# Kernel tuning notes

Measured on AMD Instinct MI355X. Metric: run time of the kernel, lower is better.

The kernel has to match this reference:

```python
import jax, jax.numpy as jnp
import numpy as np
from jax import lax

DIM = 512
HEADS = 8
N = 2048
B = 4
EPS = 1e-12  # torch F.normalize eps


def setup_inputs() -> dict:
    key = jax.random.key(0)
    ks = jax.random.split(key, 8)
    s = 0.02
    return {
        "x": jax.random.normal(ks[0], (B, DIM, N), jnp.float32),
        "w_qkv": jax.random.normal(ks[1], (3 * DIM, DIM, 1), jnp.float32) * s,
        "b_qkv": jax.random.normal(ks[2], (3 * DIM,), jnp.float32) * s,
        "w_dw": jax.random.normal(ks[3], (3 * DIM, 1, 3), jnp.float32) * s,
        "b_dw": jax.random.normal(ks[4], (3 * DIM,), jnp.float32) * s,
        "w_po": jax.random.normal(ks[5], (DIM, DIM, 1), jnp.float32) * s,
        "b_po": jax.random.normal(ks[6], (DIM,), jnp.float32) * s,
        "temperature": jnp.ones((HEADS, 1, 1), jnp.float32),
    }


def _l2norm(x, axis):
    n = jnp.sqrt(jnp.sum(x * x, axis=axis, keepdims=True))
    return x / jnp.maximum(n, EPS)


def reference(x, w_qkv, b_qkv, w_dw, b_dw, w_po, b_po, temperature):
    b, c, n = x.shape
    ch = c // HEADS
    # 1x1 conv (pointwise)
    qkv = jnp.einsum('oc,bcn->bon', w_qkv[:, :, 0], x) + b_qkv[None, :, None]
    # depthwise conv k=3, pad=1
    qkv = lax.conv_general_dilated(
        qkv, w_dw, window_strides=(1,), padding=[(1, 1)],
        dimension_numbers=('NCH', 'OIH', 'NCH'),
        feature_group_count=3 * c) + b_dw[None, :, None]
    q, k, v = jnp.split(qkv, 3, axis=1)  # each [b, c, n]
    q = q.reshape(b, HEADS, ch, n)
    k = k.reshape(b, HEADS, ch, n)
    v = v.reshape(b, HEADS, ch, n)
    q = _l2norm(q, axis=-1)          # normalize over sequence axis
    k = _l2norm(k, axis=1)           # normalize over HEAD axis (faithful)
    # attn[i, j] = sum_c k[c, i] * q[c, j]  -> [b, h, n, n]
    attn = jnp.einsum('bhci,bhcj->bhij', k, q) * temperature[None]
    attn = jax.nn.softmax(attn, axis=-1)
    out = jnp.einsum('bhij,bhcj->bhic', attn, v)  # [b, h, n, ch]
    out = out.transpose(0, 1, 3, 2).reshape(b, c, n)  # b (head c) n
    out = jnp.einsum('oc,bcn->bon', w_po[:, :, 0], out) + b_po[None, :, None]
    return out
```

## Files before the change

### kernel.cpp

```cpp
#include <hip/hip_runtime.h>
#include <hip/hip_bf16.h>

#define BATCH 4
#define DIM 512
#define HEADS 8
#define CH 64
#define SEQ 2048
#define C3 1536
#define L2EPS 1e-12f

typedef float f32x4 __attribute__((ext_vector_type(4)));
typedef short s16x8 __attribute__((ext_vector_type(8)));
typedef unsigned short ushort_t;

static __device__ __forceinline__ unsigned bfpair(float a, float b) {
  unsigned ua = __builtin_bit_cast(unsigned, a);
  unsigned ub = __builtin_bit_cast(unsigned, b);
  ua = (ua + 0x7FFFu + ((ua >> 16) & 1u)) >> 16;
  ub = (ub + 0x7FFFu + ((ub >> 16) & 1u)) >> 16;
  return ua | (ub << 16);
}

static __device__ __forceinline__ ushort_t bf16r(float a) {
  unsigned u = __builtin_bit_cast(unsigned, a);
  u = (u + 0x7FFFu + ((u >> 16) & 1u)) >> 16;
  return (ushort_t)u;
}

static __device__ __forceinline__ float bf2f(ushort_t u) {
  return __builtin_bit_cast(float, ((unsigned)u) << 16);
}

static __device__ __forceinline__ unsigned cvtpk(float lo, float hi) {
  unsigned r;
  asm("v_cvt_pk_bf16_f32 %0, %1, %2" : "=v"(r) : "v"(lo), "v"(hi));
  return r;
}

static __device__ __forceinline__ float fexp2(float x) {
  float r;
  asm("v_exp_f32 %0, %1" : "=v"(r) : "v"(x));
  return r;
}

static __device__ __forceinline__ void gl_lds16(const void* g, void* l) {
  __builtin_amdgcn_global_load_lds(
      (const __attribute__((address_space(1))) unsigned int*)g,
      (__attribute__((address_space(3))) unsigned int*)l, 16, 0, 0);
}

__global__ __launch_bounds__(256) void wprep(
    const float* __restrict__ wq, const float* __restrict__ wp,
    unsigned* __restrict__ wqb, unsigned* __restrict__ wpb) {
  const int id = blockIdx.x * 256 + threadIdx.x;
  const float* src;
  unsigned* dst;
  int rid;
  if (id < 1536 * 256) { src = wq; dst = wqb; rid = id; }
  else                 { src = wp; dst = wpb; rid = id - 1536 * 256; }
  const int m = rid >> 8, dcol = rid & 255;
  const int chunk = dcol >> 5, dw = dcol & 31;
  const int sdw = chunk * 32 + (dw ^ (4 * (m & 7)));
  const float* s = src + (size_t)m * 512 + 2 * sdw;
  dst[rid] = bfpair(s[0], s[1]);
}

__global__ __launch_bounds__(256) void xpose_bf16(
    const float* __restrict__ x, unsigned* __restrict__ xbt) {
  __shared__ unsigned T[64][32];
  const int b = blockIdx.z;
  const int k0 = blockIdx.y * 64;
  const int n0 = blockIdx.x * 64;
  const int nl = threadIdx.x & 63;
  const int dwg = threadIdx.x >> 6;
  const float* xb = x + ((size_t)b * DIM + k0) * SEQ + n0 + nl;
#pragma unroll
  for (int dd = 0; dd < 8; ++dd) {
    const int dw = dwg * 8 + dd;
    const float v0 = xb[(size_t)(2 * dw) * SEQ];
    const float v1 = xb[(size_t)(2 * dw + 1) * SEQ];
    T[nl][dw ^ (4 * (nl & 7))] = bfpair(v0, v1);
  }
  __syncthreads();
#pragma unroll
  for (int rep = 0; rep < 8; ++rep) {
    const int id = rep * 256 + threadIdx.x;
    const int row = id >> 5, dw = id & 31;
    xbt[((size_t)b * SEQ + n0 + row) * 256 + (k0 >> 1) + dw] = T[row][dw];
  }
}

template <bool OBF>
__global__ __launch_bounds__(256) void gemm_mfma_bf16(
    const ushort_t* __restrict__ Wb, const ushort_t* __restrict__ Bt,
    const float* __restrict__ bias, float* __restrict__ Y,
    int M, int N) {
  __shared__ __align__(16) char lds[32768];
  char* As = lds;
  char* Bs = lds + 16384;
  const int b = blockIdx.z;
  const int m0 = blockIdx.y * 128, n0 = blockIdx.x * 128;
  const int t = threadIdx.x, w = t >> 6, lane = t & 63;
  const int l15 = lane & 15, g = lane >> 4;
  const int key = 16 * (l15 & 7);
  const int wm = (w >> 1) * 64, wn = (w & 1) * 64;

  const int rsub = lane >> 3;
  const int csub = (lane & 7) * 8;

  f32x4 acc[4][4] = {};

  const ushort_t* Ag0 = Wb + (size_t)(m0 + 32 * w + rsub) * 512 + csub;
  const ushort_t* Bg0 = Bt + ((size_t)b * N + n0 + 32 * w + rsub) * 512 + csub;
  char* Al0 = As + (32 * w) * 128;
  char* Bl0 = Bs + (32 * w) * 128;

  for (int kc = 0; kc < 8; ++kc) {
    const int ko64 = kc * 64;
#pragma unroll
    for (int ri = 0; ri < 4; ++ri) {
      gl_lds16(Ag0 + (size_t)(8 * ri) * 512 + ko64, Al0 + ri * 1024);
      gl_lds16(Bg0 + (size_t)(8 * ri) * 512 + ko64, Bl0 + ri * 1024);
    }
    __syncthreads();
    const char* Abase = As + (wm + l15) * 128;
    const char* Bbase = Bs + (wn + l15) * 128;
#pragma unroll
    for (int ks = 0; ks < 2; ++ks) {
      const int ko = (64 * ks + 16 * g) ^ key;
      s16x8 af[4], bf[4];
#pragma unroll
      for (int mf = 0; mf < 4; ++mf) af[mf] = *(const s16x8*)(Abase + mf * 2048 + ko);
#pragma unroll
      for (int nf = 0; nf < 4; ++nf) bf[nf] = *(const s16x8*)(Bbase + nf * 2048 + ko);
#pragma unroll
      for (int mf = 0; mf < 4; ++mf)
#pragma unroll
        for (int nf = 0; nf < 4; ++nf)
          acc[mf][nf] = __builtin_amdgcn_mfma_f32_16x16x32_bf16(
              af[mf], bf[nf], acc[mf][nf], 0, 0, 0);
    }
    __syncthreads();
  }

#pragma unroll
  for (int mf = 0; mf < 4; ++mf) {
#pragma unroll
    for (int rg = 0; rg < 4; ++rg) {
      const int m = m0 + wm + 16 * mf + 4 * g + rg;
      const float bv = bias[m];
      if constexpr (OBF) {
        ushort_t* yp =
            (ushort_t*)Y + ((size_t)b * M + m) * N + n0 + wn + l15;
#pragma unroll
        for (int nf = 0; nf < 4; ++nf)
          yp[16 * nf] = bf16r(acc[mf][nf][rg] + bv);
      } else {
        float* yp = Y + ((size_t)b * M + m) * N + n0 + wn + l15;
#pragma unroll
        for (int nf = 0; nf < 4; ++nf)
          yp[16 * nf] = acc[mf][nf][rg] + bv;
      }
    }
  }
}

__global__ __launch_bounds__(256) void dwconv2(
    const ushort_t* __restrict__ pre, const float* __restrict__ wdw,
    const float* __restrict__ bdw, ushort_t* __restrict__ qkv,
    unsigned* __restrict__ vb, float* __restrict__ rq) {
  __shared__ float red[4];
  const int row = blockIdx.x;
  const int o = row % C3;
  const int b = row / C3;
  const int n0 = threadIdx.x * 8;
  const ushort_t* src = pre + (size_t)row * SEQ + n0;
  const s16x8 mv = *(const s16x8*)src;
  const float left  = (n0 > 0) ? bf2f(src[-1]) : 0.f;
  const float right = (n0 < SEQ - 8) ? bf2f(src[8]) : 0.f;
  const float w0 = wdw[o * 3 + 0], w1 = wdw[o * 3 + 1], w2 = wdw[o * 3 + 2];
  const float bv = bdw[o];
  float mid[8];
#pragma unroll
  for (int u = 0; u < 8; ++u) mid[u] = bf2f((ushort_t)mv[u]);
  const float lf[8] = {left,   mid[0], mid[1], mid[2],
                       mid[3], mid[4], mid[5], mid[6]};
  const float rt[8] = {mid[1], mid[2], mid[3], mid[4],
                       mid[5], mid[6], mid[7], right};
  float y[8];
#pragma unroll
  for (int u = 0; u < 8; ++u) y[u] = w0 * lf[u] + w1 * mid[u] + w2 * rt[u] + bv;

  if (o < 2 * DIM) {
    uint4 pk;
    pk.x = bfpair(y[0], y[1]); pk.y = bfpair(y[2], y[3]);
    pk.z = bfpair(y[4], y[5]); pk.w = bfpair(y[6], y[7]);
    *(uint4*)(qkv + (size_t)row * SEQ + n0) = pk;
    if (o < DIM) {
      float s = 0.f;
#pragma unroll
      for (int u = 0; u < 8; ++u) s += y[u] * y[u];
#pragma unroll
      for (int off = 32; off > 0; off >>= 1) s += __shfl_down(s, off);
      if ((threadIdx.x & 63) == 0) red[threadIdx.x >> 6] = s;
      __syncthreads();
      if (threadIdx.x == 0) {
        const float tv = red[0] + red[1] + red[2] + red[3];
        rq[b * DIM + o] = 1.0f / fmaxf(sqrtf(tv), L2EPS);
      }
    }
  } else {
    const int oc = o - 2 * DIM;
    const int h = oc >> 6, cc = oc & 63;
    const int bh = b * 8 + h;
    const int jt = n0 >> 6, d0 = (n0 & 63) >> 1;
    uint4 pk;
    pk.x = bfpair(y[0], y[1]); pk.y = bfpair(y[2], y[3]);
    pk.z = bfpair(y[4], y[5]); pk.w = bfpair(y[6], y[7]);
    *(uint4*)&vb[((size_t)(bh * 32 + jt) * 64 + cc) * 32 +
                 (d0 ^ (4 * (cc & 7)))] = pk;
  }
}

__global__ __launch_bounds__(256) void knorm_kernel(
    const ushort_t* __restrict__ qkv, float* __restrict__ rk) {
  const int idx = blockIdx.x * 256 + threadIdx.x;
  const int n = idx & (SEQ - 1);
  const int cc = (idx >> 11) & 63;
  const int b = idx >> 17;
  const ushort_t* base = qkv + ((size_t)b * C3 + DIM + cc) * SEQ + n;
  float s = 0.f;
#pragma unroll
  for (int h = 0; h < HEADS; ++h) {
    float v = bf2f(base[(size_t)h * CH * SEQ]);
    s += v * v;
  }
  rk[idx] = 1.0f / fmaxf(sqrtf(s), L2EPS);
}

__global__ __launch_bounds__(256) void prep2(
    const ushort_t* __restrict__ qkv, const float* __restrict__ rq,
    const float* __restrict__ rk, const float* __restrict__ temp,
    unsigned* __restrict__ qt, unsigned* __restrict__ kt) {
  __shared__ unsigned T[64][32];
  const int jt = blockIdx.x, bh = blockIdx.y, sec = blockIdx.z;
  const int b = bh >> 3, h = bh & 7;
  const int jl = threadIdx.x & 63, dwg = threadIdx.x >> 6;
  const int j = jt * 64 + jl;
  if (sec == 0) {
    const ushort_t* base = qkv + ((size_t)b * C3 + h * CH) * SEQ + j;
    const float* rqb = rq + b * DIM + h * CH;
#pragma unroll
    for (int dd = 0; dd < 8; ++dd) {
      const int dw = dwg * 8 + dd;
      float v0 = bf2f(base[(size_t)(2 * dw) * SEQ]) * rqb[2 * dw];
      float v1 = bf2f(base[(size_t)(2 * dw + 1) * SEQ]) * rqb[2 * dw + 1];
      T[jl][dw ^ (4 * (jl & 7))] = bfpair(v0, v1);
    }
  } else {
    const float f = temp[h] * 1.44269504f;
    const ushort_t* base = qkv + ((size_t)b * C3 + DIM + h * CH) * SEQ + j;
    const float* rkb = rk + (size_t)b * CH * SEQ + j;
#pragma unroll
    for (int dd = 0; dd < 8; ++dd) {
      const int dw = dwg * 8 + dd;
      float v0 = bf2f(base[(size_t)(2 * dw) * SEQ]) *
                 rkb[(size_t)(2 * dw) * SEQ] * f;
      float v1 = bf2f(base[(size_t)(2 * dw + 1) * SEQ]) *
                 rkb[(size_t)(2 * dw + 1) * SEQ] * f;
      T[jl][dw ^ (4 * (jl & 7))] = bfpair(v0, v1);
    }
  }
  __syncthreads();
  unsigned* dst = (sec == 0 ? qt : kt) + ((size_t)bh * SEQ + jt * 64) * 32;
#pragma unroll
  for (int rep = 0; rep < 8; ++rep) {
    const int id = rep * 256 + threadIdx.x;
    const int row = id >> 5, dw = id & 31;
    const unsigned val = T[row][dw ^ (4 * (row & 7))];
    if (sec == 0) {
      const int s = row >> 5, rl = row & 31;
      const int dr = (s << 5) | (16 * ((rl >> 2) & 1) + 4 * (rl >> 3) + (rl & 3));
      dst[dr * 32 + (dw ^ (4 * (dr & 7)))] = val;
    } else {
      dst[row * 32 + dw] = val;
    }
  }
}

__global__ __launch_bounds__(256, 2) void flash_mfma(
    const ushort_t* __restrict__ qt, const ushort_t* __restrict__ kt,
    const ushort_t* __restrict__ vb, unsigned* __restrict__ attn_t) {
  __shared__ __align__(16) char lds[32768];
  char* const Q0 = lds;
  char* const Q1 = lds + 8192;
  char* const V0 = lds + 16384;
  char* const V1 = lds + 24576;

  const int orig = blockIdx.y * 16 + blockIdx.x;
  const int swz = (orig & 7) * 64 + (orig >> 3);
  const int bh = swz >> 4, b = bh >> 3, h = bh & 7;
  const int i0 = (swz & 15) * 128;

  const int t = threadIdx.x, w = t >> 6, lane = t & 63;
  const int l15 = lane & 15, g = lane >> 4;
  const int key = 16 * (lane & 7);

  const ushort_t* ktp =
      kt + ((size_t)bh * SEQ + i0 + 32 * w + l15) * 64 + 8 * g;
  s16x8 kf0[2], kf1[2];
#pragma unroll
  for (int ib = 0; ib < 2; ++ib) {
    kf0[ib] = *(const s16x8*)(ktp + ib * 1024);
    kf1[ib] = *(const s16x8*)(ktp + ib * 1024 + 32);
  }

  const ushort_t* qtile = qt + (size_t)bh * SEQ * 64;
  const ushort_t* vtile = vb + (size_t)bh * 32 * 4096;

  const int li0 = (w * 2) * 64 + lane;
  const int li1 = li0 + 64;
  const int wo = (w * 2) * 1024;

  f32x4 accO[4][2] = {};
  float lr[2] = {};

#define FSTAGE(JT, QD, VD)                                               \
  do {                                                                   \
    gl_lds16(qtile + (size_t)(JT) * 4096 + li0 * 8, (QD) + wo);          \
    gl_lds16(qtile + (size_t)(JT) * 4096 + li1 * 8, (QD) + wo + 1024);   \
    gl_lds16(vtile + (size_t)(JT) * 4096 + li0 * 8, (VD) + wo);          \
    gl_lds16(vtile + (size_t)(JT) * 4096 + li1 * 8, (VD) + wo + 1024);   \
  } while (0)

  auto compute = [&](const char* Qs, const char* Vs) {
    f32x4 st[4][2];
    __builtin_amdgcn_s_setprio(1);
#pragma unroll
    for (int jf = 0; jf < 4; ++jf) {
      const char* qrow = Qs + (16 * jf + l15) * 128;
      s16x8 a0 = *(const s16x8*)(qrow + ((16 * g) ^ key));
      s16x8 a1 = *(const s16x8*)(qrow + ((16 * g + 64) ^ key));
#pragma unroll
      for (int ib = 0; ib < 2; ++ib) {
        f32x4 z = {};
        z = __builtin_amdgcn_mfma_f32_16x16x32_bf16(a0, kf0[ib], z, 0, 0, 0);
        z = __builtin_amdgcn_mfma_f32_16x16x32_bf16(a1, kf1[ib], z, 0, 0, 0);
        st[jf][ib] = z;
      }
    }
    __builtin_amdgcn_s_setprio(0);

    s16x8 pb[2][2];
#pragma unroll
    for (int ib = 0; ib < 2; ++ib)
#pragma unroll
      for (int ks = 0; ks < 2; ++ks) {
        const float e0 = fexp2(st[2 * ks][ib][0]);
        const float e1 = fexp2(st[2 * ks][ib][1]);
        const float e2 = fexp2(st[2 * ks][ib][2]);
        const float e3 = fexp2(st[2 * ks][ib][3]);
        const float e4 = fexp2(st[2 * ks + 1][ib][0]);
        const float e5 = fexp2(st[2 * ks + 1][ib][1]);
        const float e6 = fexp2(st[2 * ks + 1][ib][2]);
        const float e7 = fexp2(st[2 * ks + 1][ib][3]);
        lr[ib] += ((e0 + e1) + (e2 + e3)) + ((e4 + e5) + (e6 + e7));
        uint4 u;
        u.x = cvtpk(e0, e1);
        u.y = cvtpk(e2, e3);
        u.z = cvtpk(e4, e5);
        u.w = cvtpk(e6, e7);
        pb[ib][ks] = __builtin_bit_cast(s16x8, u);
      }

    __builtin_amdgcn_s_setprio(1);
#pragma unroll
    for (int ks = 0; ks < 2; ++ks)
#pragma unroll
      for (int mf = 0; mf < 4; ++mf) {
        const char* vrow = Vs + (16 * mf + l15) * 128;
        s16x8 aV = *(const s16x8*)(vrow + ((16 * g + 64 * ks) ^ key));
#pragma unroll
        for (int ib = 0; ib < 2; ++ib)
          accO[mf][ib] = __builtin_amdgcn_mfma_f32_16x16x32_bf16(
              aV, pb[ib][ks], accO[mf][ib], 0, 0, 0);
      }
    __builtin_amdgcn_s_setprio(0);
  };

  FSTAGE(0, Q0, V0);
  __syncthreads();
#pragma unroll 1
  for (int jt2 = 0; jt2 < 16; ++jt2) {
    const int jt = 2 * jt2;
    FSTAGE(jt + 1, Q1, V1);
    compute(Q0, V0);
    __syncthreads();
    if (jt2 < 15) FSTAGE(jt + 2, Q0, V0);
    compute(Q1, V1);
    __syncthreads();
  }

  float inv[2];
#pragma unroll
  for (int ib = 0; ib < 2; ++ib) {
    lr[ib] += __shfl_xor(lr[ib], 16);
    lr[ib] += __shfl_xor(lr[ib], 32);
    inv[ib] = 1.0f / lr[ib];
  }

  unsigned* Pw = (unsigned*)(lds + w * 4096);
  const int kk = 4 * (l15 & 7);
#pragma unroll
  for (int ib = 0; ib < 2; ++ib)
#pragma unroll
    for (int mf = 0; mf < 4; ++mf) {
      uint2 pk;
      pk.x = cvtpk(accO[mf][ib][0] * inv[ib], accO[mf][ib][1] * inv[ib]);
      pk.y = cvtpk(accO[mf][ib][2] * inv[ib], accO[mf][ib][3] * inv[ib]);
      const int dwb = 8 * mf + 2 * g;
      *(uint2*)&Pw[(16 * ib + l15) * 32 + (dwb ^ kk)] = pk;
    }
  __syncthreads();
#pragma unroll
  for (int rep = 0; rep < 16; ++rep) {
    const int id = rep * 64 + lane;
    const int row = id >> 5, dw = id & 31;
    attn_t[((size_t)b * SEQ + i0 + 32 * w + row) * 256 + h * 32 + dw] =
        Pw[row * 32 + dw];
  }
#undef FSTAGE
}

extern "C" void kernel_launch(void* const* d_in, const int* in_sizes, int n_in,
                              void* d_out, int out_size, void* d_ws, size_t ws_size,
                              hipStream_t stream) {
  const float* x      = (const float*)d_in[0];
  const float* w_qkv  = (const float*)d_in[1];
  const float* b_qkv  = (const float*)d_in[2];
  const float* w_dw   = (const float*)d_in[3];
  const float* b_dw   = (const float*)d_in[4];
  const float* w_po   = (const float*)d_in[5];
  const float* b_po   = (const float*)d_in[6];
  const float* temp   = (const float*)d_in[7];
  float* out = (float*)d_out;
  float* ws  = (float*)d_ws;

  ushort_t* qkv_pre_b = (ushort_t*)ws;
  ushort_t* qkvb = (ushort_t*)(ws + 12582912);
  float* rq      = ws + 25165824;
  float* rk      = ws + 25167872;
  unsigned* xbt  = (unsigned*)(ws + 25692160);
  unsigned* wqb  = (unsigned*)(ws + 27789312);
  unsigned* wpb  = (unsigned*)(ws + 28182528);
  unsigned* vb     = (unsigned*)(ws + 25692160);
  unsigned* qt     = (unsigned*)(ws);
  unsigned* kt     = (unsigned*)(ws + 2097152);
  unsigned* attn_t = (unsigned*)(ws + 4194304);

  wprep<<<2048, 256, 0, stream>>>(w_qkv, w_po, wqb, wpb);
  xpose_bf16<<<dim3(SEQ / 64, DIM / 64, BATCH), 256, 0, stream>>>(x, xbt);

  gemm_mfma_bf16<true><<<dim3(SEQ / 128, C3 / 128, BATCH), 256, 0, stream>>>(
      (const ushort_t*)wqb, (const ushort_t*)xbt, b_qkv,
      (float*)qkv_pre_b, C3, SEQ);

  dwconv2<<<BATCH * C3, 256, 0, stream>>>(qkv_pre_b, w_dw, b_dw, qkvb, vb, rq);

  knorm_kernel<<<(BATCH * CH * SEQ) / 256, 256, 0, stream>>>(qkvb, rk);

  prep2<<<dim3(32, BATCH * HEADS, 2), 256, 0, stream>>>(
      qkvb, rq, rk, temp, qt, kt);

  flash_mfma<<<dim3(SEQ / 128, BATCH * HEADS), 256, 0, stream>>>(
      (const ushort_t*)qt, (const ushort_t*)kt, (const ushort_t*)vb, attn_t);

  gemm_mfma_bf16<false><<<dim3(SEQ / 128, DIM / 128, BATCH), 256, 0, stream>>>(
      (const ushort_t*)wpb, (const ushort_t*)attn_t, b_po, out, DIM, SEQ);
}
```

Baseline: 111.5 us.

## Merge prep kernels and double flash attention K/V staging depth per sync

Fuses the weight-conversion and x-transpose kernels into a single launch, removing one kernel launch. In the flash attention kernel, each pipeline stage now loads two j-tiles at once into a 64KB LDS buffer, which halves the number of barriers. V fragments are also preloaded into registers before the QK MFMAs so LDS reads overlap with compute. The larger LDS footprint (64KB per block, with launch bounds asking for 2 blocks/CU) and the extra registers may reduce occupancy.

```diff
diff --git a/kernel.cpp b/kernel.cpp
--- a/kernel.cpp
+++ b/kernel.cpp
@@ -49,44 +49,45 @@
       (__attribute__((address_space(3))) unsigned int*)l, 16, 0, 0);
 }
 
-__global__ __launch_bounds__(256) void wprep(
-    const float* __restrict__ wq, const float* __restrict__ wp,
+__global__ __launch_bounds__(256) void prep_inputs(
+    const float* __restrict__ x, const float* __restrict__ wq,
+    const float* __restrict__ wp, unsigned* __restrict__ xbt,
     unsigned* __restrict__ wqb, unsigned* __restrict__ wpb) {
-  const int id = blockIdx.x * 256 + threadIdx.x;
-  const float* src;
-  unsigned* dst;
-  int rid;
-  if (id < 1536 * 256) { src = wq; dst = wqb; rid = id; }
-  else                 { src = wp; dst = wpb; rid = id - 1536 * 256; }
-  const int m = rid >> 8, dcol = rid & 255;
-  const int chunk = dcol >> 5, dw = dcol & 31;
-  const int sdw = chunk * 32 + (dw ^ (4 * (m & 7)));
-  const float* s = src + (size_t)m * 512 + 2 * sdw;
-  dst[rid] = bfpair(s[0], s[1]);
-}
-
-__global__ __launch_bounds__(256) void xpose_bf16(
-    const float* __restrict__ x, unsigned* __restrict__ xbt) {
   __shared__ unsigned T[64][32];
-  const int b = blockIdx.z;
-  const int k0 = blockIdx.y * 64;
-  const int n0 = blockIdx.x * 64;
-  const int nl = threadIdx.x & 63;
-  const int dwg = threadIdx.x >> 6;
-  const float* xb = x + ((size_t)b * DIM + k0) * SEQ + n0 + nl;
-#pragma unroll
-  for (int dd = 0; dd < 8; ++dd) {
-    const int dw = dwg * 8 + dd;
-    const float v0 = xb[(size_t)(2 * dw) * SEQ];
-    const float v1 = xb[(size_t)(2 * dw + 1) * SEQ];
-    T[nl][dw ^ (4 * (nl & 7))] = bfpair(v0, v1);
-  }
-  __syncthreads();
-#pragma unroll
-  for (int rep = 0; rep < 8; ++rep) {
-    const int id = rep * 256 + threadIdx.x;
-    const int row = id >> 5, dw = id & 31;
-    xbt[((size_t)b * SEQ + n0 + row) * 256 + (k0 >> 1) + dw] = T[row][dw];
+  const int bid = blockIdx.x;
+  if (bid < 1024) {
+    const int xx = bid & 31, ky = (bid >> 5) & 7, b = bid >> 8;
+    const int k0 = ky * 64;
+    const int n0 = xx * 64;
+    const int nl = threadIdx.x & 63;
+    const int dwg = threadIdx.x >> 6;
+    const float* xb = x + ((size_t)b * DIM + k0) * SEQ + n0 + nl;
+#pragma unroll
+    for (int dd = 0; dd < 8; ++dd) {
+      const int dw = dwg * 8 + dd;
+      const float v0 = xb[(size_t)(2 * dw) * SEQ];
+      const float v1 = xb[(size_t)(2 * dw + 1) * SEQ];
+      T[nl][dw ^ (4 * (nl & 7))] = bfpair(v0, v1);
+    }
+    __syncthreads();
+#pragma unroll
+    for (int rep = 0; rep < 8; ++rep) {
+      const int id = rep * 256 + threadIdx.x;
+      const int row = id >> 5, dw = id & 31;
+      xbt[((size_t)b * SEQ + n0 + row) * 256 + (k0 >> 1) + dw] = T[row][dw];
+    }
+  } else {
+    const int id = (bid - 1024) * 256 + threadIdx.x;
+    const float* src;
+    unsigned* dst;
+    int rid;
+    if (id < 1536 * 256) { src = wq; dst = wqb; rid = id; }
+    else                 { src = wp; dst = wpb; rid = id - 1536 * 256; }
+    const int m = rid >> 8, dcol = rid & 255;
+    const int chunk = dcol >> 5, dw = dcol & 31;
+    const int sdw = chunk * 32 + (dw ^ (4 * (m & 7)));
+    const float* s = src + (size_t)m * 512 + 2 * sdw;
+    dst[rid] = bfpair(s[0], s[1]);
   }
 }
 
@@ -291,11 +292,11 @@
 __global__ __launch_bounds__(256, 2) void flash_mfma(
     const ushort_t* __restrict__ qt, const ushort_t* __restrict__ kt,
     const ushort_t* __restrict__ vb, unsigned* __restrict__ attn_t) {
-  __shared__ __align__(16) char lds[32768];
-  char* const Q0 = lds;
-  char* const Q1 = lds + 8192;
-  char* const V0 = lds + 16384;
-  char* const V1 = lds + 24576;
+  __shared__ __align__(16) char lds[65536];
+  char* const QA = lds;
+  char* const QB = lds + 16384;
+  char* const VA = lds + 32768;
+  char* const VB = lds + 49152;
 
   const int orig = blockIdx.y * 16 + blockIdx.x;
   const int swz = (orig & 7) * 64 + (orig >> 3);
@@ -325,15 +326,29 @@
   f32x4 accO[4][2] = {};
   float lr[2] = {};
 
-#define FSTAGE(JT, QD, VD)                                               \
-  do {                                                                   \
-    gl_lds16(qtile + (size_t)(JT) * 4096 + li0 * 8, (QD) + wo);          \
-    gl_lds16(qtile + (size_t)(JT) * 4096 + li1 * 8, (QD) + wo + 1024);   \
-    gl_lds16(vtile + (size_t)(JT) * 4096 + li0 * 8, (VD) + wo);          \
-    gl_lds16(vtile + (size_t)(JT) * 4096 + li1 * 8, (VD) + wo + 1024);   \
+#define FSTAGE2(JT, QD, VD)                                               \
+  do {                                                                    \
+    gl_lds16(qtile + (size_t)(JT) * 4096 + li0 * 8, (QD) + wo);           \
+    gl_lds16(qtile + (size_t)(JT) * 4096 + li1 * 8, (QD) + wo + 1024);    \
+    gl_lds16(qtile + (size_t)(JT + 1) * 4096 + li0 * 8, (QD) + 8192 + wo);\
+    gl_lds16(qtile + (size_t)(JT + 1) * 4096 + li1 * 8,                   \
+             (QD) + 8192 + wo + 1024);                                    \
+    gl_lds16(vtile + (size_t)(JT) * 4096 + li0 * 8, (VD) + wo);           \
+    gl_lds16(vtile + (size_t)(JT) * 4096 + li1 * 8, (VD) + wo + 1024);    \
+    gl_lds16(vtile + (size_t)(JT + 1) * 4096 + li0 * 8, (VD) + 8192 + wo);\
+    gl_lds16(vtile + (size_t)(JT + 1) * 4096 + li1 * 8,                   \
+             (VD) + 8192 + wo + 1024);                                    \
   } while (0)
 
   auto compute = [&](const char* Qs, const char* Vs) {
+    s16x8 vf[2][4];
+#pragma unroll
+    for (int ks = 0; ks < 2; ++ks)
+#pragma unroll
+      for (int mf = 0; mf < 4; ++mf)
+        vf[ks][mf] = *(const s16x8*)(Vs + (16 * mf + l15) * 128 +
+                                     ((16 * g + 64 * ks) ^ key));
+
     f32x4 st[4][2];
     __builtin_amdgcn_s_setprio(1);
 #pragma unroll
@@ -377,27 +392,26 @@
 #pragma unroll
     for (int ks = 0; ks < 2; ++ks)
 #pragma unroll
-      for (int mf = 0; mf < 4; ++mf) {
-        const char* vrow = Vs + (16 * mf + l15) * 128;
-        s16x8 aV = *(const s16x8*)(vrow + ((16 * g + 64 * ks) ^ key));
+      for (int mf = 0; mf < 4; ++mf)
 #pragma unroll
         for (int ib = 0; ib < 2; ++ib)
           accO[mf][ib] = __builtin_amdgcn_mfma_f32_16x16x32_bf16(
-              aV, pb[ib][ks], accO[mf][ib], 0, 0, 0);
-      }
+              vf[ks][mf], pb[ib][ks], accO[mf][ib], 0, 0, 0);
     __builtin_amdgcn_s_setprio(0);
   };
 
-  FSTAGE(0, Q0, V0);
+  FSTAGE2(0, QA, VA);
   __syncthreads();
 #pragma unroll 1
-  for (int jt2 = 0; jt2 < 16; ++jt2) {
-    const int jt = 2 * jt2;
-    FSTAGE(jt + 1, Q1, V1);
-    compute(Q0, V0);
+  for (int s = 0; s < 8; ++s) {
+    const int t4 = 4 * s;
+    FSTAGE2(t4 + 2, QB, VB);
+    compute(QA, VA);
+    compute(QA + 8192, VA + 8192);
     __syncthreads();
-    if (jt2 < 15) FSTAGE(jt + 2, Q0, V0);
-    compute(Q1, V1);
+    if (s < 7) FSTAGE2(t4 + 4, QA, VA);
+    compute(QB, VB);
+    compute(QB + 8192, VB + 8192);
     __syncthreads();
   }
 
@@ -429,7 +443,7 @@
     attn_t[((size_t)b * SEQ + i0 + 32 * w + row) * 256 + h * 32 + dw] =
         Pw[row * 32 + dw];
   }
-#undef FSTAGE
+#undef FSTAGE2
 }
 
 extern "C" void kernel_launch(void* const* d_in, const int* in_sizes, int n_in,
@@ -458,8 +472,7 @@
   unsigned* kt     = (unsigned*)(ws + 2097152);
   unsigned* attn_t = (unsigned*)(ws + 4194304);
 
-  wprep<<<2048, 256, 0, stream>>>(w_qkv, w_po, wqb, wpb);
-  xpose_bf16<<<dim3(SEQ / 64, DIM / 64, BATCH), 256, 0, stream>>>(x, xbt);
+  prep_inputs<<<3072, 256, 0, stream>>>(x, w_qkv, w_po, xbt, wqb, wpb);
 
   gemm_mfma_bf16<true><<<dim3(SEQ / 128, C3 / 128, BATCH), 256, 0, stream>>>(
       (const ushort_t*)wqb, (const ushort_t*)xbt, b_qkv,
```

Measured after the change: 106.1 us. 1.05x faster.
